# Kernel optimization log

Hardware: AMD Instinct MI355X
Metric: run time of the kernel (lower is better)

Reference implementation:

```python
import jax, jax.numpy as jnp
import numpy as np
from jax import lax

EPS = 1e-5
F_IN, F_OUT, R = 128, 256, 16
B, H, W = 16, 128, 128


def _conv(x, w, stride):
    # x: [B,C,H,W], w: [O,I,kh,kw]; ME convs keep coordinates -> SAME padding
    return lax.conv_general_dilated(x, w, (stride, stride), 'SAME',
                                    dimension_numbers=('NCHW', 'OIHW', 'NCHW'))


def _bn(x, g, b, m, v):
    scale = g * lax.rsqrt(v + EPS)
    return x * scale[None, :, None, None] + (b - m * scale)[None, :, None, None]


def setup_inputs() -> dict:
    key = jax.random.key(0)
    ks = jax.random.split(key, 12)
    d = {}
    d['x'] = jax.random.normal(ks[0], (B, F_IN, H, W), jnp.float32)
    # BatchNorm params (eval mode running stats)
    d['bn1_g'] = jax.random.uniform(ks[1], (F_IN,), jnp.float32, 0.5, 1.5)
    d['bn1_b'] = jax.random.normal(ks[2], (F_IN,), jnp.float32) * 0.1
    d['bn1_m'] = jax.random.normal(ks[3], (F_IN,), jnp.float32) * 0.1
    d['bn1_v'] = jax.random.uniform(ks[4], (F_IN,), jnp.float32, 0.5, 1.5)
    d['bn2_g'] = jax.random.uniform(ks[5], (F_OUT,), jnp.float32, 0.5, 1.5)
    d['bn2_b'] = jax.random.normal(ks[6], (F_OUT,), jnp.float32) * 0.1
    d['bn2_m'] = jax.random.normal(ks[7], (F_OUT,), jnp.float32) * 0.1
    d['bn2_v'] = jax.random.uniform(ks[8], (F_OUT,), jnp.float32, 0.5, 1.5)
    # Conv weights (no bias, ME default)
    d['w_conv1'] = jax.random.normal(ks[9], (F_OUT, F_IN, 3, 3), jnp.float32) * (1.0 / np.sqrt(9 * F_IN))
    d['w_conv2'] = jax.random.normal(ks[10], (F_OUT, F_OUT, 3, 3), jnp.float32) * (1.0 / np.sqrt(9 * F_OUT))
    d['w_res'] = jax.random.normal(ks[11], (F_OUT, F_IN, 1, 1), jnp.float32) * (1.0 / np.sqrt(F_IN))
    # SE block linears
    k12, k13, k14, k15 = jax.random.split(jax.random.fold_in(key, 1), 4)
    d['se_w1'] = jax.random.normal(k12, (F_OUT // R, F_OUT), jnp.float32) * (1.0 / np.sqrt(F_OUT))
    d['se_b1'] = jax.random.normal(k13, (F_OUT // R,), jnp.float32) * 0.01
    d['se_w2'] = jax.random.normal(k14, (F_OUT, F_OUT // R), jnp.float32) * (1.0 / np.sqrt(F_OUT // R))
    d['se_b2'] = jax.random.normal(k15, (F_OUT,), jnp.float32) * 0.01
    return d


def reference(x, bn1_g, bn1_b, bn1_m, bn1_v, bn2_g, bn2_b, bn2_m, bn2_v,
              w_conv1, w_conv2, w_res, se_w1, se_b1, se_w2, se_b2):
    # shared BN+ReLU prefix (self.first_batch / self.first_relu reused)
    pre = jax.nn.relu(_bn(x, bn1_g, bn1_b, bn1_m, bn1_v))
    # residual branch: 1x1 stride-2 conv (f_out > f_in)
    residual = _conv(pre, w_res, 2)
    # main branch
    h = _conv(pre, w_conv1, 2)                          # [B,F_OUT,H/2,W/2]
    h = jax.nn.relu(_bn(h, bn2_g, bn2_b, bn2_m, bn2_v))
    h = _conv(h, w_conv2, 1)
    # SE attention: global avg pool -> FC -> ReLU -> FC -> sigmoid -> scale
    s = jnp.mean(h, axis=(2, 3))                        # [B,F_OUT]
    a = jax.nn.sigmoid(jax.nn.relu(s @ se_w1.T + se_b1) @ se_w2.T + se_b2)
    h = h * a[:, :, None, None]
    return h + residual
```

## Files before the change

kernel.cpp:

```cpp
#include <hip/hip_runtime.h>

typedef unsigned short u16;
typedef __attribute__((ext_vector_type(8))) unsigned short u16x8;
typedef __attribute__((ext_vector_type(8))) __bf16 bf16x8;
typedef __attribute__((ext_vector_type(4))) float f32x4;

__device__ __forceinline__ float bf2f(u16 u) {
    return __uint_as_float(((unsigned)u) << 16);
}
__device__ __forceinline__ u16 f2bf(float f) {
    unsigned u = __float_as_uint(f);
    return (u16)((u + 0x7FFFu + ((u >> 16) & 1u)) >> 16);
}

__global__ __launch_bounds__(256)
void setup_kernel(const float* __restrict__ x,
                  const float* __restrict__ g1, const float* __restrict__ b1,
                  const float* __restrict__ m1, const float* __restrict__ v1,
                  const float* __restrict__ w1, const float* __restrict__ w2,
                  const float* __restrict__ wr,
                  const float* __restrict__ g2, const float* __restrict__ b2,
                  const float* __restrict__ m2, const float* __restrict__ v2,
                  u16* __restrict__ w1t, u16* __restrict__ w2t,
                  u16* __restrict__ wrt, float* __restrict__ bias2f,
                  u16* __restrict__ pre, u16* __restrict__ h1) {
    __shared__ u16 tile[64 * 136];
    __shared__ float scf[128], bif[128];
    int b = blockIdx.x;
    int tid = threadIdx.x;
    if (b < 4096) {
        int n = b >> 8, rem = b & 255;
        int y = rem >> 1, xh = (rem & 1) << 6;
        const int lx = tid & 15;
        const int cg = tid >> 4;
        const int x4 = lx << 2;
        const int sw = lx << 3;
        const float* xb = x + (n << 21) + (y << 7) + xh + x4;
        float4 v0 = *(const float4*)(xb + ((0 * 16 + cg) << 14));
        float4 v1r = *(const float4*)(xb + ((1 * 16 + cg) << 14));
        float4 v2r = *(const float4*)(xb + ((2 * 16 + cg) << 14));
        float4 v3 = *(const float4*)(xb + ((3 * 16 + cg) << 14));
        float4 v4 = *(const float4*)(xb + ((4 * 16 + cg) << 14));
        float4 v5 = *(const float4*)(xb + ((5 * 16 + cg) << 14));
        float4 v6 = *(const float4*)(xb + ((6 * 16 + cg) << 14));
        float4 v7 = *(const float4*)(xb + ((7 * 16 + cg) << 14));
        if (tid < 128) {
            float sc = g1[tid] * rsqrtf(v1[tid] + 1e-5f);
            scf[tid] = sc;
            bif[tid] = b1[tid] - m1[tid] * sc;
        }
        __syncthreads();
#define PUT(I, V) {                                                        \
        int c = (I) * 16 + cg;                                             \
        float sc = scf[c], bi = bif[c];                                    \
        int col = c ^ sw;                                                  \
        tile[(x4 + 0) * 136 + col] = f2bf(fmaxf((V).x * sc + bi, 0.f));    \
        tile[(x4 + 1) * 136 + col] = f2bf(fmaxf((V).y * sc + bi, 0.f));    \
        tile[(x4 + 2) * 136 + col] = f2bf(fmaxf((V).z * sc + bi, 0.f));    \
        tile[(x4 + 3) * 136 + col] = f2bf(fmaxf((V).w * sc + bi, 0.f)); }
        PUT(0, v0) PUT(1, v1r) PUT(2, v2r) PUT(3, v3)
        PUT(4, v4) PUT(5, v5) PUT(6, v6) PUT(7, v7)
#undef PUT
        __syncthreads();
        int c0 = (tid & 15) << 3;
        int xo = tid >> 4;
#pragma unroll
        for (int xi = 0; xi < 4; ++xi) {
            int xloc = xi * 16 + xo;
            int colb = c0 ^ ((xloc >> 2) << 3);
            u16x8 val = *(const u16x8*)&tile[xloc * 136 + colb];
            *(u16x8*)(pre + ((n * 129 + y) * 129 + xh + xloc) * 128 + c0) = val;
        }
    } else if (b < 4096 + 3585) {
        int i = (b - 4096) * 256 + tid;
        if (i < 294912) {
            int ci = i & 127; int t = i >> 7; int o = t & 255; int tap = t >> 8;
            int dy = tap / 3, dx = tap - dy * 3;
            float sc = g2[o] * rsqrtf(v2[o] + 1e-5f);
            w1t[i] = f2bf(w1[((o * 128 + ci) * 3 + dy) * 3 + dx] * sc);
        } else if (i < 294912 + 589824) {
            int j = i - 294912;
            int ci = j & 255; int t = j >> 8; int o = t & 255; int tap = t >> 8;
            int dy = tap / 3, dx = tap - dy * 3;
            w2t[j] = f2bf(w2[((o * 256 + ci) * 3 + dy) * 3 + dx]);
        } else if (i < 294912 + 589824 + 32768) {
            int j = i - (294912 + 589824);
            int ci = j & 127; int o = j >> 7;
            wrt[j] = f2bf(wr[o * 128 + ci]);
        } else {
            int o = i - (294912 + 589824 + 32768);
            if (o < 256) {
                float sc = g2[o] * rsqrtf(v2[o] + 1e-5f);
                bias2f[o] = b2[o] - m2[o] * sc;
            }
        }
    } else if (b < 4096 + 3585 + 2056) {
        int i = (b - (4096 + 3585)) * 256 + tid;
        if (i < 16 * 129 * 128) {
            int c = i & 127; int t = i >> 7; int n = t / 129; int xx = t - n * 129;
            pre[((n * 129 + 128) * 129 + xx) * 128 + c] = 0;
        } else {
            int j = i - 16 * 129 * 128;
            int c = j & 127; int t = j >> 7; int n = t >> 7; int y = t & 127;
            pre[((n * 129 + y) * 129 + 128) * 128 + c] = 0;
        }
    } else {
        int i = (b - (4096 + 3585 + 2056)) * 256 + tid;
        int c = i & 255;
        int t = i >> 8;
        int n = t / 260;
        int cl = t - n * 260;
        int y, x2;
        if (cl < 66)       { y = 0;  x2 = cl; }
        else if (cl < 132) { y = 65; x2 = cl - 66; }
        else if (cl < 196) { x2 = 0; y = cl - 131; }
        else               { x2 = 65; y = cl - 195; }
        h1[((n * 66 + y) * 66 + x2) * 256 + c] = 0;
    }
}

template <int CIN, int NTAPS, int STRIDE, bool BIASRELU, bool POOL>
__global__ __launch_bounds__(512, 2)
void conv_8ph(const u16* __restrict__ in, const u16* __restrict__ wt,
              const float* __restrict__ bias, u16* __restrict__ out,
              float* __restrict__ pool_out,
              int in_row, int in_img, int out_base, int out_row, int out_img) {
    constexpr int CSTEPS = CIN / 64;
    constexpr int KT = CSTEPS * NTAPS;
    __shared__ __attribute__((aligned(16))) u16 lds[81920];

    const int tid = threadIdx.x;
    const int w = tid >> 6, l = tid & 63;
    const int wm = w >> 2, wn = w & 3;
    const int l15 = l & 15;
    const int bid = ((blockIdx.x & 7) << 5) | (blockIdx.x >> 3);
    const int Mbase = bid << 8;

    const int srow = tid >> 3;
    const int swze = (((tid & 7) ^ (srow & 7)) << 3);
    int pix0 = Mbase + srow;
    int nn0 = pix0 >> 12, p0 = (pix0 >> 6) & 63, q0 = pix0 & 63;
    const int abase0 = nn0 * in_img + (STRIDE * p0) * in_row + (STRIDE * q0) * CIN + swze;
    const int astep = STRIDE * in_row;
    const int bbase0 = srow * CIN + swze;
    const int bstep = 64 * CIN;

    int colw[2];
#pragma unroll
    for (int kk = 0; kk < 2; ++kk)
        colw[kk] = (kk * 32 + (l >> 4) * 8) ^ ((l & 7) << 3);

    f32x4 acc[8][4] = {};
    bf16x8 afr[4][2], bXf[2][2], bYf[2][2];

#define AOFF(ks) (((NTAPS == 9) ? ((((ks) / CSTEPS) / 3) * in_row + (((ks) / CSTEPS) % 3) * CIN) : 0) + ((ks) % CSTEPS) * 64)
#define BOFF(ks) (((ks) / CSTEPS) * 256 * CIN + ((ks) % CSTEPS) * 64)
#define GLDS(gsrc, ldst) __builtin_amdgcn_global_load_lds(                          \
        (__attribute__((address_space(1))) void*)(gsrc),                            \
        (__attribute__((address_space(3))) void*)(ldst), 16, 0, 0)
#define STAGE_A(base, h, ks) {                                                      \
    int _ao = AOFF(ks);                                                             \
    GLDS(in + abase0 + (2 * (h) + 0) * astep + _ao,                                 \
         &lds[(base) + (h) * 8192 + 0 * 4096 + w * 512]);                           \
    GLDS(in + abase0 + (2 * (h) + 1) * astep + _ao,                                 \
         &lds[(base) + (h) * 8192 + 1 * 4096 + w * 512]); }
#define STAGE_B(base, h, ks) {                                                      \
    int _bo = BOFF(ks);                                                             \
    GLDS(wt + bbase0 + (2 * (h) + 0) * bstep + _bo,                                 \
         &lds[(base) + (h) * 8192 + 0 * 4096 + w * 512]);                           \
    GLDS(wt + bbase0 + (2 * (h) + 1) * bstep + _bo,                                 \
         &lds[(base) + (h) * 8192 + 1 * 4096 + w * 512]); }
#define BARRIER() { __builtin_amdgcn_s_barrier(); asm volatile("" ::: "memory"); }
#define LDA(base, MH) {                                                             \
    _Pragma("unroll") for (int fm = 0; fm < 4; ++fm)                                \
    _Pragma("unroll") for (int kk = 0; kk < 2; ++kk)                                \
        afr[fm][kk] = *(const bf16x8*)&lds[(base) + ((MH) * 128 + wm * 64 + fm * 16 + l15) * 64 + colw[kk]]; }
#define LDB(base, NH, dst) {                                                        \
    _Pragma("unroll") for (int gn = 0; gn < 2; ++gn)                                \
    _Pragma("unroll") for (int kk = 0; kk < 2; ++kk)                                \
        dst[gn][kk] = *(const bf16x8*)&lds[(base) + ((NH) * 128 + gn * 64 + wn * 16 + l15) * 64 + colw[kk]]; }
#define MFMA_Q(MH, NH, bset) {                                                      \
    _Pragma("unroll") for (int fm = 0; fm < 4; ++fm)                                \
    _Pragma("unroll") for (int gn = 0; gn < 2; ++gn)                                \
    _Pragma("unroll") for (int kk = 0; kk < 2; ++kk)                                \
        acc[(MH) * 4 + fm][(NH) * 2 + gn] = __builtin_amdgcn_mfma_f32_16x16x32_bf16( \
            afr[fm][kk], bset[gn][kk], acc[(MH) * 4 + fm][(NH) * 2 + gn], 0, 0, 0); }

    STAGE_A(0, 0, 0); STAGE_A(0, 1, 0);
    STAGE_B(49152, 0, 0); STAGE_B(49152, 1, 0);
    STAGE_A(16384, 0, 1); STAGE_A(16384, 1, 1);
    asm volatile("s_waitcnt vmcnt(4)" ::: "memory");
    BARRIER();

    int Ar = 0;
    int As = 32768;
    int Brel = 0;

    LDB(49152, 0, bXf);

#define CBODY(T, B0, B1, STAGEA, VM)                                                \
    {                                                                               \
        const int Br = 49152 + Brel, Bs = 49152 + (Brel ^ 16384);                   \
        LDA(Ar, 0);                                                                 \
        LDB(Br, 1, B1);                                                             \
        STAGE_B(Bs, 0, (T) + 1); STAGE_B(Bs, 1, (T) + 1);                           \
        __builtin_amdgcn_s_setprio(1);                                              \
        MFMA_Q(0, 0, B0);                                                           \
        MFMA_Q(0, 1, B1);                                                           \
        __builtin_amdgcn_s_setprio(0);                                              \
        LDA(Ar, 1);                                                                 \
        if (STAGEA) { STAGE_A(As, 0, (T) + 2); STAGE_A(As, 1, (T) + 2); }           \
        __builtin_amdgcn_s_setprio(1);                                              \
        MFMA_Q(1, 1, B1);                                                           \
        __builtin_amdgcn_s_setprio(0);                                              \
        asm volatile("s_waitcnt vmcnt(" #VM ")" ::: "memory");                      \
        BARRIER();                                                                  \
        LDB(49152 + (Brel ^ 16384), 0, B1);         \
        __builtin_amdgcn_s_setprio(1);                                              \
        MFMA_Q(1, 0, B0);                                   \
        __builtin_amdgcn_s_setprio(0);                                              \
        Ar = (Ar == 32768) ? 0 : Ar + 16384;                                        \
        As = (As == 32768) ? 0 : As + 16384;                                        \
        Brel ^= 16384;                                                              \
    }

#pragma unroll 1
    for (int t = 0; t < KT - 2; t += 2) {
        CBODY(t,     bXf, bYf, true, 4);
        CBODY(t + 1, bYf, bXf, true, 4);
    }

    CBODY(KT - 2, bXf, bYf, false, 0);

    {
        const int Br = 49152 + Brel;
        LDA(Ar, 0);
        LDB(Br, 1, bXf);
        MFMA_Q(0, 0, bYf);
        MFMA_Q(0, 1, bXf);
        LDA(Ar, 1);
        MFMA_Q(1, 1, bXf);
        MFMA_Q(1, 0, bYf);
    }
#undef CBODY
#undef AOFF
#undef BOFF
#undef GLDS
#undef STAGE_A
#undef STAGE_B
#undef LDA
#undef LDB

#pragma unroll
    for (int f = 0; f < 8; ++f) {
        const int prow = (f >> 2) * 128 + wm * 64 + (f & 3) * 16 + ((l >> 4) << 2);
#pragma unroll
        for (int g = 0; g < 4; ++g) {
            const int o = (g >> 1) * 128 + (g & 1) * 64 + wn * 16 + l15;
            float bb = 0.f;
            if (BIASRELU) bb = bias[o];
#pragma unroll
            for (int j = 0; j < 4; ++j) {
                int pix = Mbase + prow + j;
                int nn = pix >> 12, p = (pix >> 6) & 63, q = pix & 63;
                float val = acc[f][g][j] + bb;
                if (BIASRELU) val = fmaxf(val, 0.f);
                out[out_base + nn * out_img + p * out_row + q * 256 + o] = f2bf(val);
            }
        }
    }

    if (POOL) {
        float ps[4];
#pragma unroll
        for (int g = 0; g < 4; ++g) {
            float s = 0.f;
#pragma unroll
            for (int f = 0; f < 8; ++f)
#pragma unroll
                for (int j = 0; j < 4; ++j) s += acc[f][g][j];
            s += __shfl_xor(s, 16);
            s += __shfl_xor(s, 32);
            ps[g] = s;
        }
        asm volatile("s_waitcnt lgkmcnt(0)" ::: "memory");
        BARRIER();
        float* fl = (float*)lds;
        if ((l >> 4) == 0) {
#pragma unroll
            for (int g = 0; g < 4; ++g) {
                int o = (g >> 1) * 128 + (g & 1) * 64 + wn * 16 + l15;
                fl[wm * 256 + o] = ps[g];
            }
        }
        BARRIER();
        if (tid < 256)
            pool_out[bid * 256 + tid] = fl[tid] + fl[256 + tid];
    }
#undef MFMA_Q
#undef BARRIER
}

__global__ __launch_bounds__(256, 2)
void finalize_kernel(const u16* __restrict__ h2, const u16* __restrict__ pre,
                     const u16* __restrict__ wrt, const float* __restrict__ part,
                     const float* __restrict__ sw1, const float* __restrict__ sb1,
                     const float* __restrict__ sw2, const float* __restrict__ sb2,
                     float* __restrict__ out) {
    __shared__ u16 th[256 * 68];
    __shared__ u16 resf[64 * 256];
    __shared__ float al[256];
    __shared__ float hl[16];
    int n = blockIdx.x >> 6, p = blockIdx.x & 63;
    int t = threadIdx.x;
    const int w = t >> 6, l = t & 63;
    const int l15 = l & 15, lk = (l >> 4) << 3;

    f32x4 racc[4][4] = {};
    {
        const u16* pbase = pre + ((n * 129 + 2 * p) * 129) * 128;
#pragma unroll
        for (int ks = 0; ks < 4; ++ks) {
            bf16x8 af[4], bf[4];
#pragma unroll
            for (int fm = 0; fm < 4; ++fm) {
                int q = fm * 16 + l15;
                af[fm] = *(const bf16x8*)(pbase + (2 * q) * 128 + ks * 32 + lk);
            }
#pragma unroll
            for (int fn = 0; fn < 4; ++fn) {
                int o = w * 64 + fn * 16 + l15;
                bf[fn] = *(const bf16x8*)(wrt + o * 128 + ks * 32 + lk);
            }
#pragma unroll
            for (int fm = 0; fm < 4; ++fm)
#pragma unroll
                for (int fn = 0; fn < 4; ++fn)
                    racc[fm][fn] = __builtin_amdgcn_mfma_f32_16x16x32_bf16(
                        af[fm], bf[fn], racc[fm][fn], 0, 0, 0);
        }
#pragma unroll
        for (int fm = 0; fm < 4; ++fm)
#pragma unroll
            for (int fn = 0; fn < 4; ++fn)
#pragma unroll
                for (int j = 0; j < 4; ++j)
                    resf[(fm * 16 + ((l >> 4) << 2) + j) * 256 + w * 64 + fn * 16 + l15] =
                        f2bf(racc[fm][fn][j]);
    }

    {
        float s = 0.f;
#pragma unroll
        for (int k = 0; k < 16; ++k) s += part[(n * 16 + k) * 256 + t];
        al[t] = s * (1.0f / 4096.0f);
    }
    __syncthreads();
    if (t < 16) {
        float d = sb1[t];
        for (int c = 0; c < 256; ++c) d += al[c] * sw1[t * 256 + c];
        hl[t] = fmaxf(d, 0.f);
    }
    __syncthreads();
    {
        float z = sb2[t];
#pragma unroll
        for (int j = 0; j < 16; ++j) z += hl[j] * sw2[t * 16 + j];
        float a_t = 1.0f / (1.0f + expf(-z));
        __syncthreads();
        al[t] = a_t;
    }
    __syncthreads();

    int o8 = (t & 31) << 3, qr = t >> 5;
    int pixbase = n * 4096 + p * 64;
#pragma unroll
    for (int qi = 0; qi < 8; ++qi) {
        int q = qi * 8 + qr;
        u16x8 hv = *(const u16x8*)(h2 + (pixbase + q) * 256 + o8);
        u16x8 rv = *(const u16x8*)(resf + q * 256 + o8);
#pragma unroll
        for (int k = 0; k < 8; ++k) {
            float vv = bf2f(hv[k]) * al[o8 + k] + bf2f(rv[k]);
            th[(o8 + k) * 68 + q] = f2bf(vv);
        }
    }
    __syncthreads();
    int q4 = (t & 15) << 2, ob = t >> 4;
#pragma unroll
    for (int oi = 0; oi < 16; ++oi) {
        int o = oi * 16 + ob;
        float4 vv;
        vv.x = bf2f(th[o * 68 + q4 + 0]);
        vv.y = bf2f(th[o * 68 + q4 + 1]);
        vv.z = bf2f(th[o * 68 + q4 + 2]);
        vv.w = bf2f(th[o * 68 + q4 + 3]);
        *(float4*)(out + ((n * 256 + o) * 64 + p) * 64 + q4) = vv;
    }
}

static const size_t OFF_PRE  = 0;
static const size_t OFF_H1   = 68161536;
static const size_t OFF_H2   = 103845888;
static const size_t OFF_W1T  = 137400320;
static const size_t OFF_W2T  = 137990144;
static const size_t OFF_WRT  = 139169792;
static const size_t OFF_B2F  = 139235328;
static const size_t OFF_PART = 139236352;

extern "C" void kernel_launch(void* const* d_in, const int* in_sizes, int n_in,
                              void* d_out, int out_size, void* d_ws, size_t ws_size,
                              hipStream_t stream) {
    (void)in_sizes; (void)n_in; (void)out_size; (void)ws_size;
    const float* x      = (const float*)d_in[0];
    const float* bn1_g  = (const float*)d_in[1];
    const float* bn1_b  = (const float*)d_in[2];
    const float* bn1_m  = (const float*)d_in[3];
    const float* bn1_v  = (const float*)d_in[4];
    const float* bn2_g  = (const float*)d_in[5];
    const float* bn2_b  = (const float*)d_in[6];
    const float* bn2_m  = (const float*)d_in[7];
    const float* bn2_v  = (const float*)d_in[8];
    const float* wc1    = (const float*)d_in[9];
    const float* wc2    = (const float*)d_in[10];
    const float* wres   = (const float*)d_in[11];
    const float* se_w1  = (const float*)d_in[12];
    const float* se_b1  = (const float*)d_in[13];
    const float* se_w2  = (const float*)d_in[14];
    const float* se_b2  = (const float*)d_in[15];

    char* ws = (char*)d_ws;
    u16*   pre    = (u16*)(ws + OFF_PRE);
    u16*   h1     = (u16*)(ws + OFF_H1);
    u16*   h2     = (u16*)(ws + OFF_H2);
    u16*   w1t    = (u16*)(ws + OFF_W1T);
    u16*   w2t    = (u16*)(ws + OFF_W2T);
    u16*   wrt    = (u16*)(ws + OFF_WRT);
    float* bias2f = (float*)(ws + OFF_B2F);
    float* part   = (float*)(ws + OFF_PART);
    float* out    = (float*)d_out;

    setup_kernel<<<13897, 256, 0, stream>>>(x, bn1_g, bn1_b, bn1_m, bn1_v,
                                            wc1, wc2, wres, bn2_g, bn2_b, bn2_m, bn2_v,
                                            w1t, w2t, wrt, bias2f, pre, h1);

    conv_8ph<128, 9, 2, true, false><<<256, 512, 0, stream>>>(
        pre, w1t, bias2f, h1, nullptr,
        129 * 128, 129 * 129 * 128,
        67 * 256, 66 * 256, 66 * 66 * 256);

    conv_8ph<256, 9, 1, false, true><<<256, 512, 0, stream>>>(
        h1, w2t, nullptr, h2, part,
        66 * 256, 66 * 66 * 256,
        0, 64 * 256, 4096 * 256);

    finalize_kernel<<<1024, 256, 0, stream>>>(h2, pre, wrt, part,
                                              se_w1, se_b1, se_w2, se_b2, out);
}
```

Baseline: 189.5 us.

## Load conv weight fragments directly from global memory instead of staging via LDS

Removes the LDS staging buffers and staging loads for the weight (B) operand in the implicit-GEMM conv kernel. Each wave now reads its B fragments straight from global memory into registers every K step. This also shrinks the shared memory footprint and simplifies the double-buffered B schedule. In exchange, global load latency is exposed inside each iteration behind a vmcnt wait, and B data is fetched redundantly by the waves that share the same columns.

```diff
diff --git a/kernel.cpp b/kernel.cpp
--- a/kernel.cpp
+++ b/kernel.cpp
@@ -127,7 +127,7 @@
               int in_row, int in_img, int out_base, int out_row, int out_img) {
     constexpr int CSTEPS = CIN / 64;
     constexpr int KT = CSTEPS * NTAPS;
-    __shared__ __attribute__((aligned(16))) u16 lds[81920];
+    __shared__ __attribute__((aligned(16))) u16 lds[49152];
 
     const int tid = threadIdx.x;
     const int w = tid >> 6, l = tid & 63;
@@ -142,8 +142,13 @@
     int nn0 = pix0 >> 12, p0 = (pix0 >> 6) & 63, q0 = pix0 & 63;
     const int abase0 = nn0 * in_img + (STRIDE * p0) * in_row + (STRIDE * q0) * CIN + swze;
     const int astep = STRIDE * in_row;
-    const int bbase0 = srow * CIN + swze;
-    const int bstep = 64 * CIN;
+
+    int bglb[4];
+#pragma unroll
+    for (int nh = 0; nh < 2; ++nh)
+#pragma unroll
+        for (int gn = 0; gn < 2; ++gn)
+            bglb[nh * 2 + gn] = (nh * 128 + gn * 64 + wn * 16 + l15) * CIN + ((l >> 4) << 3);
 
     int colw[2];
 #pragma unroll
@@ -151,7 +156,7 @@
         colw[kk] = (kk * 32 + (l >> 4) * 8) ^ ((l & 7) << 3);
 
     f32x4 acc[8][4] = {};
-    bf16x8 afr[4][2], bXf[2][2], bYf[2][2];
+    bf16x8 afr[4][2], b0f[2][2], b1f[2][2];
 
 #define AOFF(ks) (((NTAPS == 9) ? ((((ks) / CSTEPS) / 3) * in_row + (((ks) / CSTEPS) % 3) * CIN) : 0) + ((ks) % CSTEPS) * 64)
 #define BOFF(ks) (((ks) / CSTEPS) * 256 * CIN + ((ks) % CSTEPS) * 64)
@@ -164,21 +169,15 @@
          &lds[(base) + (h) * 8192 + 0 * 4096 + w * 512]);                           \
     GLDS(in + abase0 + (2 * (h) + 1) * astep + _ao,                                 \
          &lds[(base) + (h) * 8192 + 1 * 4096 + w * 512]); }
-#define STAGE_B(base, h, ks) {                                                      \
-    int _bo = BOFF(ks);                                                             \
-    GLDS(wt + bbase0 + (2 * (h) + 0) * bstep + _bo,                                 \
-         &lds[(base) + (h) * 8192 + 0 * 4096 + w * 512]);                           \
-    GLDS(wt + bbase0 + (2 * (h) + 1) * bstep + _bo,                                 \
-         &lds[(base) + (h) * 8192 + 1 * 4096 + w * 512]); }
 #define BARRIER() { __builtin_amdgcn_s_barrier(); asm volatile("" ::: "memory"); }
 #define LDA(base, MH) {                                                             \
     _Pragma("unroll") for (int fm = 0; fm < 4; ++fm)                                \
     _Pragma("unroll") for (int kk = 0; kk < 2; ++kk)                                \
         afr[fm][kk] = *(const bf16x8*)&lds[(base) + ((MH) * 128 + wm * 64 + fm * 16 + l15) * 64 + colw[kk]]; }
-#define LDB(base, NH, dst) {                                                        \
+#define BGL(NH, dst, boff) {                                                        \
     _Pragma("unroll") for (int gn = 0; gn < 2; ++gn)                                \
     _Pragma("unroll") for (int kk = 0; kk < 2; ++kk)                                \
-        dst[gn][kk] = *(const bf16x8*)&lds[(base) + ((NH) * 128 + gn * 64 + wn * 16 + l15) * 64 + colw[kk]]; }
+        dst[gn][kk] = *(const bf16x8*)(wt + bglb[(NH) * 2 + gn] + (boff) + kk * 32); }
 #define MFMA_Q(MH, NH, bset) {                                                      \
     _Pragma("unroll") for (int fm = 0; fm < 4; ++fm)                                \
     _Pragma("unroll") for (int gn = 0; gn < 2; ++gn)                                \
@@ -187,69 +186,60 @@
             afr[fm][kk], bset[gn][kk], acc[(MH) * 4 + fm][(NH) * 2 + gn], 0, 0, 0); }
 
     STAGE_A(0, 0, 0); STAGE_A(0, 1, 0);
-    STAGE_B(49152, 0, 0); STAGE_B(49152, 1, 0);
     STAGE_A(16384, 0, 1); STAGE_A(16384, 1, 1);
     asm volatile("s_waitcnt vmcnt(4)" ::: "memory");
     BARRIER();
 
     int Ar = 0;
     int As = 32768;
-    int Brel = 0;
-
-    LDB(49152, 0, bXf);
-
-#define CBODY(T, B0, B1, STAGEA, VM)                                                \
-    {                                                                               \
-        const int Br = 49152 + Brel, Bs = 49152 + (Brel ^ 16384);                   \
+
+#define CBODY(T, VM, STAGEA) {                                                      \
+        const int _bo = BOFF(T);                                                    \
+        BGL(0, b0f, _bo); BGL(1, b1f, _bo);                                         \
         LDA(Ar, 0);                                                                 \
-        LDB(Br, 1, B1);                                                             \
-        STAGE_B(Bs, 0, (T) + 1); STAGE_B(Bs, 1, (T) + 1);                           \
+        if (STAGEA) { STAGE_A(As, 0, (T) + 2); STAGE_A(As, 1, (T) + 2); }           \
+        asm volatile("s_waitcnt vmcnt(" #VM ") lgkmcnt(0)" ::: "memory");           \
         __builtin_amdgcn_s_setprio(1);                                              \
-        MFMA_Q(0, 0, B0);                                                           \
-        MFMA_Q(0, 1, B1);                                                           \
+        MFMA_Q(0, 0, b0f);                                                          \
+        MFMA_Q(0, 1, b1f);                                                          \
         __builtin_amdgcn_s_setprio(0);                                              \
         LDA(Ar, 1);                                                                 \
-        if (STAGEA) { STAGE_A(As, 0, (T) + 2); STAGE_A(As, 1, (T) + 2); }           \
+        asm volatile("s_waitcnt lgkmcnt(0)" ::: "memory");                          \
         __builtin_amdgcn_s_setprio(1);                                              \
-        MFMA_Q(1, 1, B1);                                                           \
+        MFMA_Q(1, 1, b1f);                                                          \
+        MFMA_Q(1, 0, b0f);                                                          \
         __builtin_amdgcn_s_setprio(0);                                              \
-        asm volatile("s_waitcnt vmcnt(" #VM ")" ::: "memory");                      \
         BARRIER();                                                                  \
-        LDB(49152 + (Brel ^ 16384), 0, B1);         \
-        __builtin_amdgcn_s_setprio(1);                                              \
-        MFMA_Q(1, 0, B0);                                   \
-        __builtin_amdgcn_s_setprio(0);                                              \
         Ar = (Ar == 32768) ? 0 : Ar + 16384;                                        \
         As = (As == 32768) ? 0 : As + 16384;                                        \
-        Brel ^= 16384;                                                              \
     }
 
 #pragma unroll 1
-    for (int t = 0; t < KT - 2; t += 2) {
-        CBODY(t,     bXf, bYf, true, 4);
-        CBODY(t + 1, bYf, bXf, true, 4);
-    }
-
-    CBODY(KT - 2, bXf, bYf, false, 0);
+    for (int t = 0; t < KT - 2; ++t) {
+        CBODY(t, 4, true);
+    }
+
+    CBODY(KT - 2, 0, false);
 
     {
-        const int Br = 49152 + Brel;
+        const int _bo = BOFF(KT - 1);
+        BGL(0, b0f, _bo); BGL(1, b1f, _bo);
         LDA(Ar, 0);
-        LDB(Br, 1, bXf);
-        MFMA_Q(0, 0, bYf);
-        MFMA_Q(0, 1, bXf);
+        asm volatile("s_waitcnt vmcnt(0) lgkmcnt(0)" ::: "memory");
+        MFMA_Q(0, 0, b0f);
+        MFMA_Q(0, 1, b1f);
         LDA(Ar, 1);
-        MFMA_Q(1, 1, bXf);
-        MFMA_Q(1, 0, bYf);
+        asm volatile("s_waitcnt lgkmcnt(0)" ::: "memory");
+        MFMA_Q(1, 1, b1f);
+        MFMA_Q(1, 0, b0f);
     }
 #undef CBODY
 #undef AOFF
 #undef BOFF
 #undef GLDS
 #undef STAGE_A
-#undef STAGE_B
 #undef LDA
-#undef LDB
+#undef BGL
 
 #pragma unroll
     for (int f = 0; f < 8; ++f) {
```

Measured after the change: 266.3 us. +40.5%, slower.
